# Optimization experiments

Measured on AMD Instinct MI355X. Metric: run time of the kernel, lower is better.

## Reference

```python
import jax, jax.numpy as jnp
import numpy as np

LN_EPS = 1e-5


def setup_inputs() -> dict:
    key = jax.random.key(0)
    ks = jax.random.split(key, 6)
    T, B, D, O, G = 32, 4096, 128, 128, 9
    x = jax.random.normal(ks[0], (T, B, D), dtype=jnp.float32)
    sequence_mask = jnp.ones((T, B, 1), dtype=bool)
    # freq: arange(1,G+1)/(G+1)  (norm_freq=True, is_first=False)
    freq = (jnp.arange(1, G + 1, dtype=jnp.float32) / (G + 1)).reshape(1, 1, 1, G)
    # phase buffer: grid_phase + input_phase + small perturbations
    grid_phase = jnp.linspace(0.0, np.pi, G).reshape(1, 1, 1, G)
    input_phase = jnp.linspace(0.0, np.pi, D).reshape(1, 1, D, 1)
    gp_pert = jax.random.uniform(ks[1], (1, 1, 1, G)) / G * 0.1
    ip_pert = jax.random.uniform(ks[2], (1, 1, D, 1)) / D * 0.1
    phase = (grid_phase + input_phase + gp_pert + ip_pert).astype(jnp.float32)
    # amplitudes: uniform(-1,1)/O / grid_norm_factor  -> (O, D, G)
    grid_norm = (jnp.arange(G, dtype=jnp.float32) + 1.0).reshape(1, 1, G)
    amplitudes = (jax.random.uniform(ks[3], (O, D, 1), minval=-1.0, maxval=1.0) / O) / grid_norm
    bias = jnp.ones((1, O), dtype=jnp.float32) / O
    ln_weight = jnp.ones((D,), dtype=jnp.float32)
    ln_bias = jnp.zeros((D,), dtype=jnp.float32)
    return {"x": x, "sequence_mask": sequence_mask, "freq": freq, "phase": phase,
            "amplitudes": amplitudes, "bias": bias, "ln_weight": ln_weight, "ln_bias": ln_bias}


def reference(x, sequence_mask, freq, phase, amplitudes, bias, ln_weight, ln_bias):
    T, B, D = x.shape
    O, _, G = amplitudes.shape
    # LayerNorm over feature dim
    mu = jnp.mean(x, axis=-1, keepdims=True)
    var = jnp.mean(jnp.square(x - mu), axis=-1, keepdims=True)
    xn = (x - mu) * jax.lax.rsqrt(var + LN_EPS) * ln_weight + ln_bias
    xf = xn.reshape(T * B, D)
    # sine basis expansion: (N, D, G)
    s = jnp.sin(xf[:, :, None] * freq.reshape(1, 1, G) + phase.reshape(1, D, G))
    # contraction to output dim: (N, O)
    y = jnp.einsum('nkg,okg->no', s, amplitudes) + bias
    y = y.reshape(T, B, O)
    return y * sequence_mask.astype(y.dtype)
```

## Files before the change

kernel.cpp:

```cpp
#include <hip/hip_runtime.h>
#include <hip/hip_bf16.h>

typedef __attribute__((ext_vector_type(8))) short short8;
typedef __attribute__((ext_vector_type(16))) float f32x16;
typedef __attribute__((ext_vector_type(4))) unsigned uint4v;
typedef unsigned int u32;

#define D_DIM 128
#define G_DIM 9
#define O_DIM 128
#define K_DIM 1152
#define BROWS 256
#define INV2PI 0.15915494309189535f

__device__ __forceinline__ short f2bf(float f) {
  unsigned u = __float_as_uint(f);
  unsigned r = (u + 0x7FFFu + ((u >> 16) & 1u)) >> 16;
  return (short)r;
}

__device__ __forceinline__ unsigned pk2bf(float a, float b) {
  __hip_bfloat162 h = __float22bfloat162_rn(float2{a, b});
  return *reinterpret_cast<unsigned*>(&h);
}

__global__ void sinekan_prep(const float* __restrict__ amp,
                             const float* __restrict__ phase,
                             const float* __restrict__ freq,
                             short* __restrict__ Bp,
                             float* __restrict__ pt2,
                             float* __restrict__ fq2) {
  int i = blockIdx.x * blockDim.x + threadIdx.x;
  if (i < G_DIM * O_DIM * D_DIM) {
    int g = i >> 14, rem = i & 16383, o = rem >> 7, d = rem & 127;
    Bp[(g << 14) + (o << 7) + (d ^ ((o & 7) << 3))] = f2bf(amp[(o * D_DIM + d) * G_DIM + g]);
  }
  if (i < K_DIM) {
    int g = i >> 7, d = i & 127;
    pt2[i] = phase[d * G_DIM + g] * INV2PI;
  }
  if (i < G_DIM) fq2[i] = freq[i] * INV2PI;
}

__device__ __forceinline__ void stage_b(const short* __restrict__ Bp, short* dst_lds,
                                        int g, int tid) {
  const char* src = (const char*)Bp + ((size_t)g << 15) + tid * 16;
  char* dst = (char*)dst_lds + (tid >> 6) * 1024;
#pragma unroll
  for (int c = 0; c < 8; ++c) {
    __builtin_amdgcn_global_load_lds(
        (const __attribute__((address_space(1))) u32*)(src + c * 4096),
        (__attribute__((address_space(3))) u32*)(dst + c * 4096), 16, 0, 0);
  }
}

__global__ __launch_bounds__(256, 2)
void sinekan_fused(const float* __restrict__ x,
                   const int* __restrict__ mask,
                   const float* __restrict__ bias,
                   const float* __restrict__ lnw,
                   const float* __restrict__ lnb,
                   const short* __restrict__ Bp,
                   const float* __restrict__ pt2,
                   const float* __restrict__ fq2,
                   float* __restrict__ out) {
  __shared__ short b_lds[2][O_DIM * D_DIM];
  __shared__ float pt_lds[G_DIM * D_DIM];
  __shared__ float mu_s[BROWS], rs_s[BROWS], mk_s[BROWS];
  __shared__ float w_s[D_DIM], bb_s[D_DIM];

  const int tid = threadIdx.x;
  const int row0 = blockIdx.x * BROWS;
  const int wv = tid >> 6, lane = tid & 63, lr = lane & 31, hi = lane >> 5;

  stage_b(Bp, b_lds[0], 0, tid);

  if (tid < D_DIM) { w_s[tid] = lnw[tid]; bb_s[tid] = lnb[tid]; }
  mk_s[tid] = mask[row0 + tid] ? 1.0f : 0.0f;
  for (int i = tid; i < G_DIM * D_DIM; i += 256) pt_lds[i] = pt2[i];

  {
    int rloc = tid >> 4, ch = tid & 15;
#pragma unroll 1
    for (int it = 0; it < 16; ++it) {
      int r = it * 16 + rloc;
      const float4* xp = (const float4*)(x + (size_t)(row0 + r) * D_DIM + ch * 8);
      float4 a = xp[0], b = xp[1];
      float s  = a.x + a.y + a.z + a.w + b.x + b.y + b.z + b.w;
      float sq = a.x*a.x + a.y*a.y + a.z*a.z + a.w*a.w
               + b.x*b.x + b.y*b.y + b.z*b.z + b.w*b.w;
#pragma unroll
      for (int off = 1; off < 16; off <<= 1) {
        s  += __shfl_xor(s, off, 64);
        sq += __shfl_xor(sq, off, 64);
      }
      if (ch == 0) {
        float m = s * (1.0f / 128.0f);
        mu_s[r] = m;
        rs_s[r] = rsqrtf(sq * (1.0f / 128.0f) - m * m + 1e-5f);
      }
    }
  }
  __syncthreads();

  uint4v xnc[2][8];
#pragma unroll
  for (int m = 0; m < 2; ++m) {
    const int rl = wv * 64 + m * 32 + lr;
    const float mu = mu_s[rl], rs = rs_s[rl];
    const float* xr = x + (size_t)(row0 + rl) * D_DIM;
#pragma unroll
    for (int kk = 0; kk < 8; ++kk) {
      const int d0 = kk * 16 + hi * 8;
      float4 xa = *(const float4*)(xr + d0);
      float4 xb = *(const float4*)(xr + d0 + 4);
      float xv[8] = {xa.x, xa.y, xa.z, xa.w, xb.x, xb.y, xb.z, xb.w};
      uint4v pk;
#pragma unroll
      for (int jj = 0; jj < 4; ++jj) {
        float e0 = (xv[2*jj]   - mu) * rs * w_s[d0 + 2*jj]   + bb_s[d0 + 2*jj];
        float e1 = (xv[2*jj+1] - mu) * rs * w_s[d0 + 2*jj+1] + bb_s[d0 + 2*jj+1];
        pk[jj] = pk2bf(e0, e1);
      }
      xnc[m][kk] = pk;
    }
  }
  __syncthreads();

  const int hs = ((hi << 4) ^ ((lr & 7) << 4));
  const char* blr = (const char*)&b_lds[0][0] + (lr << 8);
  const float* ptl = pt_lds + (hi << 3);

  f32x16 acc[2][4] = {};

#pragma unroll 1
  for (int g = 0; g < G_DIM; ++g) {
    if (g + 1 < G_DIM) stage_b(Bp, b_lds[(g + 1) & 1], g + 1, tid);
    const float fgv = fq2[g];
    const char* bl = blr + ((g & 1) << 15);
    const float* ptg = ptl + (g << 7);

#pragma unroll
    for (int kk = 0; kk < 8; ++kk) {
      const char* ba = bl + (((kk << 5)) ^ hs);
      short8 bf0 = *(const short8*)(ba);
      short8 bf1 = *(const short8*)(ba + 8192);
      short8 bf2 = *(const short8*)(ba + 16384);
      short8 bf3 = *(const short8*)(ba + 24576);
      float4 p0 = *(const float4*)(ptg + kk * 16);
      float4 p1 = *(const float4*)(ptg + kk * 16 + 4);

      const float ph[8] = {p0.x, p0.y, p0.z, p0.w, p1.x, p1.y, p1.z, p1.w};
      short8 af[2];
#pragma unroll
      for (int m = 0; m < 2; ++m) {
        uint4v pk;
#pragma unroll
        for (int jj = 0; jj < 4; ++jj) {
          unsigned u = xnc[m][kk][jj];
          float e0 = __uint_as_float(u << 16);
          float e1 = __uint_as_float(u & 0xffff0000u);
          float s0 = __builtin_amdgcn_sinf(fmaf(e0, fgv, ph[2*jj]));
          float s1 = __builtin_amdgcn_sinf(fmaf(e1, fgv, ph[2*jj+1]));
          pk[jj] = pk2bf(s0, s1);
        }
        af[m] = __builtin_bit_cast(short8, pk);
      }

      __builtin_amdgcn_s_setprio(1);
      acc[0][0] = __builtin_amdgcn_mfma_f32_32x32x16_bf16(af[0], bf0, acc[0][0], 0, 0, 0);
      acc[0][1] = __builtin_amdgcn_mfma_f32_32x32x16_bf16(af[0], bf1, acc[0][1], 0, 0, 0);
      acc[0][2] = __builtin_amdgcn_mfma_f32_32x32x16_bf16(af[0], bf2, acc[0][2], 0, 0, 0);
      acc[0][3] = __builtin_amdgcn_mfma_f32_32x32x16_bf16(af[0], bf3, acc[0][3], 0, 0, 0);
      acc[1][0] = __builtin_amdgcn_mfma_f32_32x32x16_bf16(af[1], bf0, acc[1][0], 0, 0, 0);
      acc[1][1] = __builtin_amdgcn_mfma_f32_32x32x16_bf16(af[1], bf1, acc[1][1], 0, 0, 0);
      acc[1][2] = __builtin_amdgcn_mfma_f32_32x32x16_bf16(af[1], bf2, acc[1][2], 0, 0, 0);
      acc[1][3] = __builtin_amdgcn_mfma_f32_32x32x16_bf16(af[1], bf3, acc[1][3], 0, 0, 0);
      __builtin_amdgcn_s_setprio(0);
    }
    __syncthreads();
  }

#pragma unroll
  for (int m = 0; m < 2; ++m) {
#pragma unroll
    for (int n = 0; n < 4; ++n) {
      int col = n * 32 + lr;
      float bv = bias[col];
#pragma unroll
      for (int reg = 0; reg < 16; ++reg) {
        int rit  = (reg & 3) + 8 * (reg >> 2) + 4 * hi;
        int rloc = wv * 64 + m * 32 + rit;
        out[(size_t)(row0 + rloc) * O_DIM + col] = (acc[m][n][reg] + bv) * mk_s[rloc];
      }
    }
  }
}

extern "C" void kernel_launch(void* const* d_in, const int* in_sizes, int n_in,
                              void* d_out, int out_size, void* d_ws, size_t ws_size,
                              hipStream_t stream) {
  const float* x    = (const float*)d_in[0];
  const int* mk     = (const int*)d_in[1];
  const float* freq = (const float*)d_in[2];
  const float* phase= (const float*)d_in[3];
  const float* amp  = (const float*)d_in[4];
  const float* bias = (const float*)d_in[5];
  const float* lnw  = (const float*)d_in[6];
  const float* lnb  = (const float*)d_in[7];
  float* out = (float*)d_out;

  int N = in_sizes[0] / D_DIM;
  short* Bp = (short*)d_ws;
  float* pt2 = (float*)((char*)d_ws + (size_t)G_DIM * O_DIM * D_DIM * sizeof(short));
  float* fq2 = pt2 + G_DIM * D_DIM;

  int total = G_DIM * O_DIM * D_DIM;
  sinekan_prep<<<(total + 255) / 256, 256, 0, stream>>>(amp, phase, freq, Bp, pt2, fq2);
  sinekan_fused<<<N / BROWS, 256, 0, stream>>>(x, mk, bias, lnw, lnb, Bp, pt2, fq2, out);
}
```

Before: 200.6 us.

## Use 512-thread blocks with one 32-row M tile per wave

Doubles the block to 512 threads so each of 8 waves handles 32 rows instead of 64, halving the accumulator and cached-activation registers per thread and adjusting B staging, LayerNorm stats and the epilogue for the new thread count. It also prefetches the next phase vector one step ahead and drops a redundant barrier. This aims to give more resident waves to hide sine and LDS latency, at the cost of each B fragment read from LDS feeding only one MFMA instead of two.

```diff
diff --git a/kernel.cpp b/kernel.cpp
--- a/kernel.cpp
+++ b/kernel.cpp
@@ -11,6 +11,7 @@
 #define O_DIM 128
 #define K_DIM 1152
 #define BROWS 256
+#define NTHR 512
 #define INV2PI 0.15915494309189535f
 
 __device__ __forceinline__ short f2bf(float f) {
@@ -47,14 +48,14 @@
   const char* src = (const char*)Bp + ((size_t)g << 15) + tid * 16;
   char* dst = (char*)dst_lds + (tid >> 6) * 1024;
 #pragma unroll
-  for (int c = 0; c < 8; ++c) {
+  for (int c = 0; c < 4; ++c) {
     __builtin_amdgcn_global_load_lds(
-        (const __attribute__((address_space(1))) u32*)(src + c * 4096),
-        (__attribute__((address_space(3))) u32*)(dst + c * 4096), 16, 0, 0);
-  }
-}
-
-__global__ __launch_bounds__(256, 2)
+        (const __attribute__((address_space(1))) u32*)(src + c * 8192),
+        (__attribute__((address_space(3))) u32*)(dst + c * 8192), 16, 0, 0);
+  }
+}
+
+__global__ __launch_bounds__(NTHR, 3)
 void sinekan_fused(const float* __restrict__ x,
                    const int* __restrict__ mask,
                    const float* __restrict__ bias,
@@ -76,14 +77,14 @@
   stage_b(Bp, b_lds[0], 0, tid);
 
   if (tid < D_DIM) { w_s[tid] = lnw[tid]; bb_s[tid] = lnb[tid]; }
-  mk_s[tid] = mask[row0 + tid] ? 1.0f : 0.0f;
-  for (int i = tid; i < G_DIM * D_DIM; i += 256) pt_lds[i] = pt2[i];
+  if (tid < BROWS) mk_s[tid] = mask[row0 + tid] ? 1.0f : 0.0f;
+  for (int i = tid; i < G_DIM * D_DIM; i += NTHR) pt_lds[i] = pt2[i];
 
   {
     int rloc = tid >> 4, ch = tid & 15;
 #pragma unroll 1
-    for (int it = 0; it < 16; ++it) {
-      int r = it * 16 + rloc;
+    for (int it = 0; it < 8; ++it) {
+      int r = it * 32 + rloc;
       const float4* xp = (const float4*)(x + (size_t)(row0 + r) * D_DIM + ch * 8);
       float4 a = xp[0], b = xp[1];
       float s  = a.x + a.y + a.z + a.w + b.x + b.y + b.z + b.w;
@@ -103,10 +104,9 @@
   }
   __syncthreads();
 
-  uint4v xnc[2][8];
-#pragma unroll
-  for (int m = 0; m < 2; ++m) {
-    const int rl = wv * 64 + m * 32 + lr;
+  uint4v xnc[8];
+  {
+    const int rl = wv * 32 + lr;
     const float mu = mu_s[rl], rs = rs_s[rl];
     const float* xr = x + (size_t)(row0 + rl) * D_DIM;
 #pragma unroll
@@ -122,16 +122,15 @@
         float e1 = (xv[2*jj+1] - mu) * rs * w_s[d0 + 2*jj+1] + bb_s[d0 + 2*jj+1];
         pk[jj] = pk2bf(e0, e1);
       }
-      xnc[m][kk] = pk;
-    }
-  }
-  __syncthreads();
-
-  const int hs = ((hi << 4) ^ ((lr & 7) << 4));
+      xnc[kk] = pk;
+    }
+  }
+
+  const int hs = (hi << 4) ^ ((lr & 7) << 4);
   const char* blr = (const char*)&b_lds[0][0] + (lr << 8);
   const float* ptl = pt_lds + (hi << 3);
 
-  f32x16 acc[2][4] = {};
+  f32x16 acc[4] = {};
 
 #pragma unroll 1
   for (int g = 0; g < G_DIM; ++g) {
@@ -140,59 +139,52 @@
     const char* bl = blr + ((g & 1) << 15);
     const float* ptg = ptl + (g << 7);
 
+    float4 p0 = *(const float4*)(ptg);
+    float4 p1 = *(const float4*)(ptg + 4);
+
 #pragma unroll
     for (int kk = 0; kk < 8; ++kk) {
-      const char* ba = bl + (((kk << 5)) ^ hs);
+      const char* ba = bl + ((kk << 5) ^ hs);
       short8 bf0 = *(const short8*)(ba);
       short8 bf1 = *(const short8*)(ba + 8192);
       short8 bf2 = *(const short8*)(ba + 16384);
       short8 bf3 = *(const short8*)(ba + 24576);
-      float4 p0 = *(const float4*)(ptg + kk * 16);
-      float4 p1 = *(const float4*)(ptg + kk * 16 + 4);
+      const int kn = (kk + 1) & 7;
+      float4 q0 = *(const float4*)(ptg + kn * 16);
+      float4 q1 = *(const float4*)(ptg + kn * 16 + 4);
 
       const float ph[8] = {p0.x, p0.y, p0.z, p0.w, p1.x, p1.y, p1.z, p1.w};
-      short8 af[2];
-#pragma unroll
-      for (int m = 0; m < 2; ++m) {
-        uint4v pk;
-#pragma unroll
-        for (int jj = 0; jj < 4; ++jj) {
-          unsigned u = xnc[m][kk][jj];
-          float e0 = __uint_as_float(u << 16);
-          float e1 = __uint_as_float(u & 0xffff0000u);
-          float s0 = __builtin_amdgcn_sinf(fmaf(e0, fgv, ph[2*jj]));
-          float s1 = __builtin_amdgcn_sinf(fmaf(e1, fgv, ph[2*jj+1]));
-          pk[jj] = pk2bf(s0, s1);
-        }
-        af[m] = __builtin_bit_cast(short8, pk);
-      }
+      uint4v pk;
+#pragma unroll
+      for (int jj = 0; jj < 4; ++jj) {
+        unsigned u = xnc[kk][jj];
+        float s0 = __builtin_amdgcn_sinf(fmaf(__uint_as_float(u << 16),         fgv, ph[2*jj]));
+        float s1 = __builtin_amdgcn_sinf(fmaf(__uint_as_float(u & 0xffff0000u), fgv, ph[2*jj+1]));
+        pk[jj] = pk2bf(s0, s1);
+      }
+      short8 af = __builtin_bit_cast(short8, pk);
 
       __builtin_amdgcn_s_setprio(1);
-      acc[0][0] = __builtin_amdgcn_mfma_f32_32x32x16_bf16(af[0], bf0, acc[0][0], 0, 0, 0);
-      acc[0][1] = __builtin_amdgcn_mfma_f32_32x32x16_bf16(af[0], bf1, acc[0][1], 0, 0, 0);
-      acc[0][2] = __builtin_amdgcn_mfma_f32_32x32x16_bf16(af[0], bf2, acc[0][2], 0, 0, 0);
-      acc[0][3] = __builtin_amdgcn_mfma_f32_32x32x16_bf16(af[0], bf3, acc[0][3], 0, 0, 0);
-      acc[1][0] = __builtin_amdgcn_mfma_f32_32x32x16_bf16(af[1], bf0, acc[1][0], 0, 0, 0);
-      acc[1][1] = __builtin_amdgcn_mfma_f32_32x32x16_bf16(af[1], bf1, acc[1][1], 0, 0, 0);
-      acc[1][2] = __builtin_amdgcn_mfma_f32_32x32x16_bf16(af[1], bf2, acc[1][2], 0, 0, 0);
-      acc[1][3] = __builtin_amdgcn_mfma_f32_32x32x16_bf16(af[1], bf3, acc[1][3], 0, 0, 0);
+      acc[0] = __builtin_amdgcn_mfma_f32_32x32x16_bf16(af, bf0, acc[0], 0, 0, 0);
+      acc[1] = __builtin_amdgcn_mfma_f32_32x32x16_bf16(af, bf1, acc[1], 0, 0, 0);
+      acc[2] = __builtin_amdgcn_mfma_f32_32x32x16_bf16(af, bf2, acc[2], 0, 0, 0);
+      acc[3] = __builtin_amdgcn_mfma_f32_32x32x16_bf16(af, bf3, acc[3], 0, 0, 0);
       __builtin_amdgcn_s_setprio(0);
+
+      p0 = q0; p1 = q1;
     }
     __syncthreads();
   }
 
 #pragma unroll
-  for (int m = 0; m < 2; ++m) {
-#pragma unroll
-    for (int n = 0; n < 4; ++n) {
-      int col = n * 32 + lr;
-      float bv = bias[col];
-#pragma unroll
-      for (int reg = 0; reg < 16; ++reg) {
-        int rit  = (reg & 3) + 8 * (reg >> 2) + 4 * hi;
-        int rloc = wv * 64 + m * 32 + rit;
-        out[(size_t)(row0 + rloc) * O_DIM + col] = (acc[m][n][reg] + bv) * mk_s[rloc];
-      }
+  for (int n = 0; n < 4; ++n) {
+    int col = n * 32 + lr;
+    float bv = bias[col];
+#pragma unroll
+    for (int reg = 0; reg < 16; ++reg) {
+      int rit  = (reg & 3) + 8 * (reg >> 2) + 4 * hi;
+      int rloc = wv * 32 + rit;
+      out[(size_t)(row0 + rloc) * O_DIM + col] = (acc[n][reg] + bv) * mk_s[rloc];
     }
   }
 }
@@ -217,5 +209,5 @@
 
   int total = G_DIM * O_DIM * D_DIM;
   sinekan_prep<<<(total + 255) / 256, 256, 0, stream>>>(amp, phase, freq, Bp, pt2, fq2);
-  sinekan_fused<<<N / BROWS, 256, 0, stream>>>(x, mk, bias, lnw, lnb, Bp, pt2, fq2, out);
-}
+  sinekan_fused<<<N / BROWS, NTHR, 0, stream>>>(x, mk, bias, lnw, lnb, Bp, pt2, fq2, out);
+}
```

Result: faster. 184.4 us (-8.1%).
